# Kernel tuning notes

Measured on AMD Instinct MI355X. Metric: run time of the kernel, lower is better.

Reference implementation:

```python
import jax, jax.numpy as jnp
import numpy as np

N, M, D = 2048, 100000, 128
K = 5


def setup_inputs() -> dict:
    key = jax.random.key(0)
    k1, k2 = jax.random.split(key)
    features = jax.random.normal(k1, (N, D), dtype=jnp.float32)
    memory_bank = jax.random.normal(k2, (M, D), dtype=jnp.float32)
    # normalization buffers computed during fit(); use plausible scalars
    min_val = jnp.zeros((), dtype=jnp.float32)
    max_val = jnp.ones((), dtype=jnp.float32)
    return {
        "features": features,
        "memory_bank": memory_bank,
        "min_val": min_val,
        "max_val": max_val,
        "n_neighbors": K,
    }


def reference(features, memory_bank, min_val, max_val, n_neighbors):
    x2 = jnp.sum(features * features, axis=1, keepdims=True)        # (N,1)
    y2 = jnp.sum(memory_bank * memory_bank, axis=1)[None, :]        # (1,M)
    d2 = x2 + y2 - 2.0 * (features @ memory_bank.T)                 # (N,M)
    dist = jnp.sqrt(jnp.maximum(d2, 0.0))
    # k smallest distances per query (topk largest=False)
    neg_knn, _ = jax.lax.top_k(-dist, n_neighbors)                  # (N,K)
    knn = -neg_knn
    # min-max normalization with fitted stats
    knn = (knn - min_val) / (max_val - min_val)
    return knn.mean(axis=1)                                         # (N,)
```

## Files before the change

### kernel.cpp

```cpp
#include <hip/hip_runtime.h>
#include <stdint.h>

#define N_Q 2048
#define M_B 100000
#define D_DIM 128
#define KNN 5
#define SLABS_TOTAL 1563
#define M_PAD (SLABS_TOTAL * 64)
#define CHUNKS 64
#define SPC 25
#define CLS 16
#define FTOT (CHUNKS * CLS)
#define ROWBLOCKS 16
#define TROWS 128
#define BIGF 3.0e38f
#define NEGF -3.0e38f


typedef __attribute__((ext_vector_type(8))) short short8;
typedef __attribute__((ext_vector_type(4))) unsigned short ushort4v;
typedef __attribute__((ext_vector_type(8))) unsigned short ushort8v;
typedef __attribute__((ext_vector_type(4))) float f32x4;

static __device__ __forceinline__ unsigned short f2bf(float f) {
  unsigned int u = __builtin_bit_cast(unsigned int, f);
  u = (u + 0x7FFFu + ((u >> 16) & 1u)) >> 16;
  return (unsigned short)u;
}

static __device__ __forceinline__ void gload_lds16(const void* g, void* l) {
  __builtin_amdgcn_global_load_lds((const __attribute__((address_space(1))) unsigned int*)g,
                                   (__attribute__((address_space(3))) unsigned int*)l, 16, 0, 0);
}
static __device__ __forceinline__ void gload_lds4(const void* g, void* l) {
  __builtin_amdgcn_global_load_lds((const __attribute__((address_space(1))) unsigned int*)g,
                                   (__attribute__((address_space(3))) unsigned int*)l, 4, 0, 0);
}

#define DPPADD(v, ctrl)                                                              \
  do {                                                                               \
    int _t = __builtin_amdgcn_update_dpp(0, __builtin_bit_cast(int, (v)), (ctrl),    \
                                         0xf, 0xf, false);                           \
    (v) = (v) + __builtin_bit_cast(float, _t);                                       \
  } while (0)

__global__ __launch_bounds__(256) void k_prep(const float* __restrict__ Y,
                                              unsigned short* __restrict__ ybf,
                                              float* __restrict__ ny2) {
  const int s = blockIdx.x;
  const int t = threadIdx.x;
  __shared__ __align__(16) unsigned short tile[8192];
  __shared__ float redy[64 * 33];
#pragma unroll
  for (int i = 0; i < 8; ++i) {
    const int u = i * 256 + t;
    const int rowl = u >> 5;
    const int q = u & 31;
    const int rowg = s * 64 + rowl;
    const int rowc = (rowg < M_B) ? rowg : (M_B - 1);
    const float4 v = ((const float4*)Y)[(size_t)rowc * 32 + q];
    redy[rowl * 33 + q] = v.x * v.x + v.y * v.y + v.z * v.z + v.w * v.w;
    ushort4v o;
    o[0] = f2bf(v.x); o[1] = f2bf(v.y); o[2] = f2bf(v.z); o[3] = f2bf(v.w);
    *(ushort4v*)(tile + (size_t)(((q >> 1) * 64 + rowl) * 8 + (q & 1) * 4)) = o;
  }
  __syncthreads();
  {
    const int rowl = t >> 2;
    const int k = t & 3;
    float ss = 0.f;
#pragma unroll
    for (int j = 0; j < 8; ++j) ss += redy[rowl * 33 + k * 8 + j];
    DPPADD(ss, 0xB1);
    DPPADD(ss, 0x4E);
    const int rowg = s * 64 + rowl;
    if ((t & 3) == 0) ny2[(size_t)s * 64 + rowl] = (rowg < M_B) ? (-0.5f * ss) : NEGF;
  }
#pragma unroll
  for (int i = 0; i < 4; ++i) {
    const int u = i * 256 + t;
    *(ushort8v*)(ybf + ((size_t)s * 1024 + u) * 8) = *(const ushort8v*)(tile + u * 8);
  }
}

__global__ __launch_bounds__(256, 4) void k_main(const float* __restrict__ X,
                                                 const unsigned short* __restrict__ ybf,
                                                 const float* __restrict__ ny2,
                                                 float* __restrict__ rsm) {
  __shared__ __align__(16) char smem[33280];
  unsigned short* ys = (unsigned short*)smem;
  float* ny2s = (float*)(smem + 32768);

  const int bid = blockIdx.x;
  const int chunk = bid % CHUNKS;
  const int rowblock = bid / CHUNKS;
  const int row0 = rowblock * TROWS;

  const int cs0 = chunk * SPC;
  int nslab = SLABS_TOTAL - cs0;
  if (nslab > SPC) nslab = SPC;

  const int t = threadIdx.x;
  const int wave = t >> 6;
  const int lane = t & 63;
  const int lm = lane & 15;
  const int lq = lane >> 4;

  short8 afrag[2][4];
#pragma unroll
  for (int rt = 0; rt < 2; ++rt)
#pragma unroll
    for (int ks = 0; ks < 4; ++ks) {
      const float* xr = X + (size_t)(row0 + wave * 32 + rt * 16 + lm) * D_DIM + ks * 32 + lq * 8;
      const float4 a = *(const float4*)xr;
      const float4 b = *(const float4*)(xr + 4);
      short8 f;
      f[0] = (short)f2bf(a.x); f[1] = (short)f2bf(a.y);
      f[2] = (short)f2bf(a.z); f[3] = (short)f2bf(a.w);
      f[4] = (short)f2bf(b.x); f[5] = (short)f2bf(b.y);
      f[6] = (short)f2bf(b.z); f[7] = (short)f2bf(b.w);
      afrag[rt][ks] = f;
    }

  float prmax[2][4];
#pragma unroll
  for (int rt = 0; rt < 2; ++rt)
#pragma unroll
    for (int rr = 0; rr < 4; ++rr) prmax[rt][rr] = NEGF;

  for (int s = 0; s < nslab; s += 2) {
    const int sg0 = cs0 + s;
    const int two = (s + 1 < nslab);
#pragma unroll
    for (int sl = 0; sl < 2; ++sl) {
      if (sl && !two) break;
      const unsigned short* src = ybf + (size_t)(sg0 + sl) * 8192;
#pragma unroll
      for (int i = 0; i < 4; ++i) {
        const int ub = i * 256 + wave * 64;
        gload_lds16(src + (size_t)(ub + lane) * 8, ys + (size_t)(sl * 8192 + ub * 8));
      }
    }
    if (wave == 0) {
      gload_lds4(ny2 + (size_t)sg0 * 64 + lane, ny2s);
      if (two) gload_lds4(ny2 + (size_t)(sg0 + 1) * 64 + lane, ny2s + 64);
    }
    __syncthreads();

#pragma unroll
    for (int sl = 0; sl < 2; ++sl) {
      if (sl && !two) break;
      float y2c[4];
#pragma unroll
      for (int ct = 0; ct < 4; ++ct) y2c[ct] = ny2s[sl * 64 + ct * 16 + lm];

      f32x4 acc[2][4];
#pragma unroll
      for (int rt = 0; rt < 2; ++rt)
#pragma unroll
        for (int ct = 0; ct < 4; ++ct)
#pragma unroll
          for (int rr = 0; rr < 4; ++rr) acc[rt][ct][rr] = y2c[ct];

#pragma unroll
      for (int ct = 0; ct < 4; ++ct) {
        short8 bfr[4];
#pragma unroll
        for (int ks = 0; ks < 4; ++ks)
          bfr[ks] = *(const short8*)(ys + (size_t)(sl * 8192 +
                       (((ks * 4 + lq) * 64 + ct * 16 + lm)) * 8));
#pragma unroll
        for (int rt = 0; rt < 2; ++rt)
#pragma unroll
          for (int ks = 0; ks < 4; ++ks)
            acc[rt][ct] = __builtin_amdgcn_mfma_f32_16x16x32_bf16(afrag[rt][ks], bfr[ks],
                                                                  acc[rt][ct], 0, 0, 0);
      }

#pragma unroll
      for (int rt = 0; rt < 2; ++rt)
#pragma unroll
        for (int rr = 0; rr < 4; ++rr) {
          const float cm = fmaxf(fmaxf(fmaxf(acc[rt][0][rr], acc[rt][1][rr]),
                                       acc[rt][2][rr]), acc[rt][3][rr]);
          prmax[rt][rr] = fmaxf(prmax[rt][rr], cm);
        }
    }
    __syncthreads();
  }

#pragma unroll
  for (int rt = 0; rt < 2; ++rt)
#pragma unroll
    for (int rr = 0; rr < 4; ++rr) {
      const int lrow = wave * 32 + rt * 16 + lq * 4 + rr;
      rsm[(size_t)(row0 + lrow) * FTOT + chunk * CLS + lm] = prmax[rt][rr];
    }
}

__global__ __launch_bounds__(256) void k_scan(const float* __restrict__ rsm,
                                              const float* __restrict__ X,
                                              const float* __restrict__ minp,
                                              const float* __restrict__ maxp,
                                              float* __restrict__ out) {
  const int wave = threadIdx.x >> 6;
  const int lane = threadIdx.x & 63;
  const int row = blockIdx.x * 4 + wave;
  const float* rp = rsm + (size_t)row * FTOT;

  float x2;
  {
    const float a = X[(size_t)row * D_DIM + lane];
    const float b = X[(size_t)row * D_DIM + 64 + lane];
    x2 = a * a + b * b;
#pragma unroll
    for (int off = 1; off < 64; off <<= 1) x2 += __shfl_xor(x2, off);
  }

  float t0 = NEGF, t1 = NEGF, t2 = NEGF, t3 = NEGF, t4 = NEGF;
  for (int i = lane; i < FTOT; i += 64) {
    const float v = rp[i];
    if (v > t4) {
      float m = v;
      float n3 = fminf(t3, m); m = fmaxf(t3, m);
      float n2 = fminf(t2, m); m = fmaxf(t2, m);
      float n1 = fminf(t1, m); m = fmaxf(t1, m);
      float n0 = fminf(t0, m); m = fmaxf(t0, m);
      t0 = m; t1 = n0; t2 = n1; t3 = n2; t4 = n3;
    }
  }

  int k = 0;
  float sum = 0.f;
#pragma unroll
  for (int r = 0; r < KNN; ++r) {
    float head = (k == 0) ? t0 : (k == 1) ? t1 : (k == 2) ? t2 : (k == 3) ? t3
               : (k == 4) ? t4 : NEGF;
    float m = head;
#pragma unroll
    for (int off = 1; off < 64; off <<= 1) m = fmaxf(m, __shfl_xor(m, off));
    const unsigned long long mask = __ballot(head == m);
    const int first = __ffsll(mask) - 1;
    if (lane == first) ++k;
    sum += sqrtf(fmaxf(x2 - 2.f * m, 0.f));
  }
  if (lane == 0) {
    const float mn = minp[0], mx = maxp[0];
    out[row] = (sum * (1.0f / KNN) - mn) / (mx - mn);
  }
}

extern "C" void kernel_launch(void* const* d_in, const int* in_sizes, int n_in,
                              void* d_out, int out_size, void* d_ws, size_t ws_size,
                              hipStream_t stream) {
  const float* X = (const float*)d_in[0];
  const float* Y = (const float*)d_in[1];
  const float* minp = (const float*)d_in[2];
  const float* maxp = (const float*)d_in[3];
  float* out = (float*)d_out;

  char* ws = (char*)d_ws;
  size_t off = 0;
  unsigned short* ybf = (unsigned short*)(ws + off); off += (size_t)M_PAD * D_DIM * 2;
  float* ny2 = (float*)(ws + off);                   off += (size_t)M_PAD * 4;
  float* rsm = (float*)(ws + off);                   off += (size_t)N_Q * FTOT * 4;

  k_prep<<<dim3(SLABS_TOTAL), dim3(256), 0, stream>>>(Y, ybf, ny2);
  k_main<<<dim3(ROWBLOCKS * CHUNKS), dim3(256), 0, stream>>>(X, ybf, ny2, rsm);
  k_scan<<<dim3(N_Q / 4), dim3(256), 0, stream>>>(rsm, X, minp, maxp, out);
}
```

Measured before the change: 148.9 us.

## Double-buffer memory-bank slabs in LDS to overlap loads with MFMA compute

```diff
diff --git a/kernel.cpp b/kernel.cpp
--- a/kernel.cpp
+++ b/kernel.cpp
@@ -87,7 +87,7 @@
                                                  const unsigned short* __restrict__ ybf,
                                                  const float* __restrict__ ny2,
                                                  float* __restrict__ rsm) {
-  __shared__ __align__(16) char smem[33280];
+  __shared__ __align__(16) char smem[39168];
   unsigned short* ys = (unsigned short*)smem;
   float* ny2s = (float*)(smem + 32768);
 
@@ -99,6 +99,7 @@
   const int cs0 = chunk * SPC;
   int nslab = SLABS_TOTAL - cs0;
   if (nslab > SPC) nslab = SPC;
+  if (nslab < 0) nslab = 0;
 
   const int t = threadIdx.x;
   const int wave = t >> 6;
@@ -122,71 +123,79 @@
       afrag[rt][ks] = f;
     }
 
+  for (int j = wave; j < nslab; j += 4)
+    gload_lds4(ny2 + (size_t)(cs0 + j) * 64 + lane, ny2s + (size_t)j * 64);
+  __syncthreads();
+
   float prmax[2][4];
 #pragma unroll
   for (int rt = 0; rt < 2; ++rt)
 #pragma unroll
     for (int rr = 0; rr < 4; ++rr) prmax[rt][rr] = NEGF;
 
-  for (int s = 0; s < nslab; s += 2) {
-    const int sg0 = cs0 + s;
-    const int two = (s + 1 < nslab);
-#pragma unroll
-    for (int sl = 0; sl < 2; ++sl) {
-      if (sl && !two) break;
-      const unsigned short* src = ybf + (size_t)(sg0 + sl) * 8192;
+  if (nslab > 0) {
+    const unsigned short* src = ybf + (size_t)cs0 * 8192;
+#pragma unroll
+    for (int i = 0; i < 4; ++i) {
+      const int ub = i * 256 + wave * 64;
+      gload_lds16(src + (size_t)(ub + lane) * 8, ys + (size_t)ub * 8);
+    }
+  }
+
+  for (int s = 0; s < nslab; ++s) {
+    unsigned short* yb = ys + (size_t)(s & 1) * 8192;
+    if (s + 1 < nslab) {
+      const unsigned short* src = ybf + (size_t)(cs0 + s + 1) * 8192;
+      unsigned short* dst = ys + (size_t)((s + 1) & 1) * 8192;
 #pragma unroll
       for (int i = 0; i < 4; ++i) {
         const int ub = i * 256 + wave * 64;
-        gload_lds16(src + (size_t)(ub + lane) * 8, ys + (size_t)(sl * 8192 + ub * 8));
+        gload_lds16(src + (size_t)(ub + lane) * 8, dst + (size_t)ub * 8);
       }
-    }
-    if (wave == 0) {
-      gload_lds4(ny2 + (size_t)sg0 * 64 + lane, ny2s);
-      if (two) gload_lds4(ny2 + (size_t)(sg0 + 1) * 64 + lane, ny2s + 64);
-    }
-    __syncthreads();
-
-#pragma unroll
-    for (int sl = 0; sl < 2; ++sl) {
-      if (sl && !two) break;
-      float y2c[4];
-#pragma unroll
-      for (int ct = 0; ct < 4; ++ct) y2c[ct] = ny2s[sl * 64 + ct * 16 + lm];
-
-      f32x4 acc[2][4];
+      asm volatile("s_waitcnt vmcnt(4)" ::: "memory");
+    } else {
+      asm volatile("s_waitcnt vmcnt(0)" ::: "memory");
+    }
+    __builtin_amdgcn_s_barrier();
+
+    float y2c[4];
+#pragma unroll
+    for (int ct = 0; ct < 4; ++ct) y2c[ct] = ny2s[s * 64 + ct * 16 + lm];
+
+    f32x4 acc[2][4];
+#pragma unroll
+    for (int rt = 0; rt < 2; ++rt)
+#pragma unroll
+      for (int ct = 0; ct < 4; ++ct)
+#pragma unroll
+        for (int rr = 0; rr < 4; ++rr) acc[rt][ct][rr] = y2c[ct];
+
+    __builtin_amdgcn_s_setprio(1);
+#pragma unroll
+    for (int ct = 0; ct < 4; ++ct) {
+      short8 bfr[4];
+#pragma unroll
+      for (int ks = 0; ks < 4; ++ks)
+        bfr[ks] = *(const short8*)(yb + (size_t)(((ks * 4 + lq) * 64 + ct * 16 + lm)) * 8);
 #pragma unroll
       for (int rt = 0; rt < 2; ++rt)
 #pragma unroll
-        for (int ct = 0; ct < 4; ++ct)
-#pragma unroll
-          for (int rr = 0; rr < 4; ++rr) acc[rt][ct][rr] = y2c[ct];
-
-#pragma unroll
-      for (int ct = 0; ct < 4; ++ct) {
-        short8 bfr[4];
-#pragma unroll
         for (int ks = 0; ks < 4; ++ks)
-          bfr[ks] = *(const short8*)(ys + (size_t)(sl * 8192 +
-                       (((ks * 4 + lq) * 64 + ct * 16 + lm)) * 8));
-#pragma unroll
-        for (int rt = 0; rt < 2; ++rt)
-#pragma unroll
-          for (int ks = 0; ks < 4; ++ks)
-            acc[rt][ct] = __builtin_amdgcn_mfma_f32_16x16x32_bf16(afrag[rt][ks], bfr[ks],
-                                                                  acc[rt][ct], 0, 0, 0);
+          acc[rt][ct] = __builtin_amdgcn_mfma_f32_16x16x32_bf16(afrag[rt][ks], bfr[ks],
+                                                                acc[rt][ct], 0, 0, 0);
+    }
+    __builtin_amdgcn_s_setprio(0);
+
+#pragma unroll
+    for (int rt = 0; rt < 2; ++rt)
+#pragma unroll
+      for (int rr = 0; rr < 4; ++rr) {
+        const float cm = fmaxf(fmaxf(fmaxf(acc[rt][0][rr], acc[rt][1][rr]),
+                                     acc[rt][2][rr]), acc[rt][3][rr]);
+        prmax[rt][rr] = fmaxf(prmax[rt][rr], cm);
       }
 
-#pragma unroll
-      for (int rt = 0; rt < 2; ++rt)
-#pragma unroll
-        for (int rr = 0; rr < 4; ++rr) {
-          const float cm = fmaxf(fmaxf(fmaxf(acc[rt][0][rr], acc[rt][1][rr]),
-                                       acc[rt][2][rr]), acc[rt][3][rr]);
-          prmax[rt][rr] = fmaxf(prmax[rt][rr], cm);
-        }
-    }
-    __syncthreads();
+    __builtin_amdgcn_s_barrier();
   }
 
 #pragma unroll
```

Measured after the change: 146.7 us. About the same (-1.4%).
